# Kernel optimization log

Measured on AMD Instinct MI355X. Metric: run time of the kernel, lower is better.

Reference implementation:

```python
import jax, jax.numpy as jnp
import numpy as np

D_MODEL, D_FF, N_EXPERTS, TOP_K = 1024, 4096, 8, 2
B, S = 2, 2048


def setup_inputs() -> dict:
    key = jax.random.key(0)
    ks = jax.random.split(key, 7)
    scale = 0.02
    return {
        "x": jax.random.normal(ks[0], (B, S, D_MODEL), dtype=jnp.float32),
        "W1": jax.random.normal(ks[1], (N_EXPERTS, D_MODEL, D_FF), dtype=jnp.float32) * scale,
        "b1": jnp.zeros((N_EXPERTS, D_FF), dtype=jnp.float32),
        "W2": jax.random.normal(ks[2], (N_EXPERTS, D_FF, D_MODEL), dtype=jnp.float32) * scale,
        "b2": jnp.zeros((N_EXPERTS, D_MODEL), dtype=jnp.float32),
        "Wg": jax.random.normal(ks[3], (D_MODEL, N_EXPERTS), dtype=jnp.float32) * scale,
        "bg": jnp.zeros((N_EXPERTS,), dtype=jnp.float32),
    }


def reference(x, W1, b1, W2, b2, Wg, bg):
    # x: [B, S, d_model]
    Bx, Sx, d = x.shape
    E = W1.shape[0]
    # Gate + top-k routing (softmax over the top-k scores, as in the torch code)
    logits = jnp.einsum("bsd,de->bse", x, Wg) + bg            # [B,S,E]
    topk_scores, topk_idx = jax.lax.top_k(logits, TOP_K)       # [B,S,K]
    topk_scores = jax.nn.softmax(topk_scores, axis=-1)

    tokens = x.reshape(-1, d)                                  # [T,d]
    idx_flat = topk_idx.reshape(-1, TOP_K)                     # [T,K]
    sc_flat = topk_scores.reshape(-1, TOP_K)                   # [T,K]
    # Per-token combine weight for each expert: sum_k score_k * 1[idx_k == e]
    comb = (jax.nn.one_hot(idx_flat, E, dtype=x.dtype) * sc_flat[..., None]).sum(axis=1)  # [T,E]

    # Dense grouped expert MLP (zero combine weight kills non-selected experts)
    h = jnp.einsum("td,edf->etf", tokens, W1) + b1[:, None, :]  # [E,T,d_ff]
    even = (jnp.arange(E) % 2 == 0)[:, None, None]
    # torch nn.GELU default = exact (erf); odd experts use SiLU
    a = jnp.where(even, jax.nn.gelu(h, approximate=False), jax.nn.silu(h))
    y = jnp.einsum("etf,efd->etd", a, W2) + b2[:, None, :]      # [E,T,d_model]
    out = jnp.einsum("te,etd->td", comb, y)                     # [T,d_model]
    # Dropout is identity in eval mode
    return out.reshape(Bx, Sx, d)
```

## Files before the change

### kernel.cpp

```cpp
#include <hip/hip_runtime.h>
#include <stdint.h>

#define T_TOK 4096
#define DM 1024
#define DF 4096
#define NE 8

typedef __attribute__((ext_vector_type(8))) short bf16x8;
typedef __attribute__((ext_vector_type(4))) float f32x4;

__device__ __forceinline__ float b2f(unsigned short u) {
    union { unsigned int i; float f; } v; v.i = ((unsigned int)u) << 16; return v.f;
}
__device__ __forceinline__ unsigned short f2b(float f) {
    unsigned int i = __float_as_uint(f);
    unsigned int r = (i + 0x7FFFu + ((i >> 16) & 1u)) >> 16;
    return (unsigned short)r;
}
__device__ __forceinline__ void load_lds16(const void* g, void* l) {
    __builtin_amdgcn_global_load_lds((__attribute__((address_space(1))) void*)(g),
                                     (__attribute__((address_space(3))) void*)(l), 16, 0, 0);
}

__device__ __forceinline__ float fexp2(float x) {
#if __has_builtin(__builtin_amdgcn_exp2f)
    return __builtin_amdgcn_exp2f(x);
#else
    return exp2f(x);
#endif
}
__device__ __forceinline__ float frcp(float x) {
#if __has_builtin(__builtin_amdgcn_rcpf)
    return __builtin_amdgcn_rcpf(x);
#else
    return 1.0f / x;
#endif
}

__device__ __forceinline__ float gelu_f(float h) {
    float z = h * 0.70710678118654752f;
    float az = fabsf(z);
    float t = frcp(1.0f + 0.3275911f * az);
    float p = ((((1.061405429f * t - 1.453152027f) * t + 1.421413741f) * t
                - 0.284496736f) * t + 0.254829592f) * t;
    float e = fexp2(-1.4426950408889634f * az * az);
    float er = 1.0f - p * e;
    er = (z < 0.f) ? -er : er;
    return 0.5f * h * (1.0f + er);
}
__device__ __forceinline__ float silu_f(float h) {
    return h * frcp(1.0f + fexp2(-1.4426950408889634f * h));
}

__global__ __launch_bounds__(256) void detect_kernel(const unsigned short* __restrict__ xu,
                                                     int* __restrict__ flag) {
    const int i = (blockIdx.x * 256 + threadIdx.x) * 4;
    uint2 v = *(const uint2*)&xu[i];
    unsigned int a = v.x, b = v.y;
    int found = 0;
    if (((a >> 7)  & 0xFF) == 0xFF) found = 1;
    if (((a >> 23) & 0xFF) == 0xFF) found = 1;
    if (((b >> 7)  & 0xFF) == 0xFF) found = 1;
    if (((b >> 23) & 0xFF) == 0xFF) found = 1;
    if (__ballot(found) != 0 && (threadIdx.x & 63) == 0) atomicOr(flag, 1);
}

__global__ __launch_bounds__(256) void convx_kernel(const void* __restrict__ xin,
                                                    const int* __restrict__ flag,
                                                    unsigned short* __restrict__ xb) {
    const size_t i = ((size_t)blockIdx.x * 256 + threadIdx.x) * 8;
    if (*flag) {
        const float* xf = (const float*)xin + i;
        float4 a = *(const float4*)xf;
        float4 b = *(const float4*)(xf + 4);
        alignas(16) unsigned short t[8] = { f2b(a.x), f2b(a.y), f2b(a.z), f2b(a.w),
                                            f2b(b.x), f2b(b.y), f2b(b.z), f2b(b.w) };
        *(uint4*)(xb + i) = *(const uint4*)t;
    } else {
        *(uint4*)(xb + i) = *(const uint4*)((const unsigned short*)xin + i);
    }
}

__global__ void convf_kernel(const void* __restrict__ src, const int* __restrict__ flag,
                             float* __restrict__ dst, int n) {
    int i = blockIdx.x * 256 + threadIdx.x;
    if (i < n) dst[i] = (*flag) ? ((const float*)src)[i] : b2f(((const unsigned short*)src)[i]);
}

__global__ __launch_bounds__(256) void transpose_kernel(const void* __restrict__ in,
                                                        unsigned short* __restrict__ out,
                                                        int R, int C, const int* __restrict__ flag) {
    __shared__ unsigned short tile[64][65];
    const int isf = *flag;
    const size_t base = (size_t)blockIdx.z * R * C;
    const int r0 = blockIdx.y * 64, c0 = blockIdx.x * 64;
    const int lr = threadIdx.x >> 2;
    const int lc = (threadIdx.x & 3) * 16;
    if (isf) {
        const float* src = (const float*)in + base + (size_t)(r0 + lr) * C + c0 + lc;
#pragma unroll
        for (int q = 0; q < 4; q++) {
            float4 v = *(const float4*)(src + q * 4);
            tile[lr][lc + q * 4 + 0] = f2b(v.x);
            tile[lr][lc + q * 4 + 1] = f2b(v.y);
            tile[lr][lc + q * 4 + 2] = f2b(v.z);
            tile[lr][lc + q * 4 + 3] = f2b(v.w);
        }
    } else {
        const unsigned short* src = (const unsigned short*)in + base + (size_t)(r0 + lr) * C + c0 + lc;
#pragma unroll
        for (int q = 0; q < 2; q++) {
            uint4 v = *(const uint4*)(src + q * 8);
            unsigned int w[4] = { v.x, v.y, v.z, v.w };
#pragma unroll
            for (int j = 0; j < 4; j++) {
                tile[lr][lc + q * 8 + 2 * j]     = (unsigned short)(w[j] & 0xffff);
                tile[lr][lc + q * 8 + 2 * j + 1] = (unsigned short)(w[j] >> 16);
            }
        }
    }
    __syncthreads();
    const int oc = threadIdx.x >> 2;
    const int oj = (threadIdx.x & 3) * 16;
    alignas(16) unsigned short tmp[16];
#pragma unroll
    for (int j = 0; j < 16; j++) tmp[j] = tile[oj + j][oc];
    unsigned short* dst = out + base + (size_t)(c0 + oc) * R + r0 + oj;
    *(uint4*)(dst) = *(const uint4*)(tmp);
    *(uint4*)(dst + 8) = *(const uint4*)(tmp + 8);
}

__global__ __launch_bounds__(256) void gate_kernel(
    const void* __restrict__ x, const void* __restrict__ Wg, const void* __restrict__ bg,
    const int* __restrict__ flag, int* __restrict__ cnt,
    int* __restrict__ tok_e, float* __restrict__ tok_s) {
    const int isf = *flag;
    const int wave = threadIdx.x >> 6, lane = threadIdx.x & 63;
    const int t = blockIdx.x * 4 + wave;
    float p[8] = {0.f,0.f,0.f,0.f,0.f,0.f,0.f,0.f};
    if (isf) {
        const float* xr = (const float*)x + (size_t)t * DM;
        const float* wg = (const float*)Wg;
        for (int i = lane; i < DM; i += 64) {
            float xv = xr[i];
            float4 a = *(const float4*)(wg + (size_t)i * 8);
            float4 b = *(const float4*)(wg + (size_t)i * 8 + 4);
            p[0] += xv * a.x; p[1] += xv * a.y; p[2] += xv * a.z; p[3] += xv * a.w;
            p[4] += xv * b.x; p[5] += xv * b.y; p[6] += xv * b.z; p[7] += xv * b.w;
        }
    } else {
        const unsigned short* xr = (const unsigned short*)x + (size_t)t * DM;
        const unsigned short* wg = (const unsigned short*)Wg;
        for (int i = lane; i < DM; i += 64) {
            float xv = b2f(xr[i]);
            uint4 wv = *(const uint4*)(wg + (size_t)i * 8);
            p[0] += xv * b2f((unsigned short)(wv.x & 0xffff));
            p[1] += xv * b2f((unsigned short)(wv.x >> 16));
            p[2] += xv * b2f((unsigned short)(wv.y & 0xffff));
            p[3] += xv * b2f((unsigned short)(wv.y >> 16));
            p[4] += xv * b2f((unsigned short)(wv.z & 0xffff));
            p[5] += xv * b2f((unsigned short)(wv.z >> 16));
            p[6] += xv * b2f((unsigned short)(wv.w & 0xffff));
            p[7] += xv * b2f((unsigned short)(wv.w >> 16));
        }
    }
    for (int off = 32; off > 0; off >>= 1)
        for (int e = 0; e < 8; e++) p[e] += __shfl_down(p[e], off);
    if (lane == 0) {
        for (int e = 0; e < 8; e++)
            p[e] += isf ? ((const float*)bg)[e] : b2f(((const unsigned short*)bg)[e]);
        int e0 = 0;
        for (int e = 1; e < 8; e++) if (p[e] > p[e0]) e0 = e;
        int e1 = (e0 == 0) ? 1 : 0;
        for (int e = 0; e < 8; e++) if (e != e0 && p[e] > p[e1]) e1 = e;
        float z = expf(p[e1] - p[e0]);
        float s0 = 1.f / (1.f + z);
        tok_e[2 * t] = e0; tok_e[2 * t + 1] = e1;
        tok_s[2 * t] = s0; tok_s[2 * t + 1] = z * s0;
        atomicAdd(&cnt[e0], 1); atomicAdd(&cnt[e1], 1);
    }
}

__global__ void scan_kernel(const int* __restrict__ cnt, int* __restrict__ offs) {
    if (threadIdx.x == 0) {
        int s = 0;
        for (int e = 0; e < NE; e++) { offs[e] = s; s += cnt[e]; }
    }
}

__global__ __launch_bounds__(256) void place_kernel(
    const int* __restrict__ tok_e, const int* __restrict__ offs, int* __restrict__ cnt2,
    int* __restrict__ tok_list, int* __restrict__ slot_of) {
    const int t = blockIdx.x * 256 + threadIdx.x;
    for (int k = 0; k < 2; k++) {
        int e = tok_e[2 * t + k];
        int slot = atomicAdd(&cnt2[e], 1);
        int idx = offs[e] + slot;
        tok_list[idx] = t;
        slot_of[2 * t + k] = idx;
    }
}

__global__ __launch_bounds__(256) void gemm1_kernel(
    const unsigned short* __restrict__ xb, const unsigned short* __restrict__ W1T,
    const float* __restrict__ b1f, const int* __restrict__ tok_list,
    const int* __restrict__ offs, const int* __restrict__ cnt,
    unsigned short* __restrict__ act) {
    const int e = blockIdx.z, by = blockIdx.y, bx = blockIdx.x;
    const int ne = cnt[e];
    if (by * 128 >= ne) return;
    const int off_e = offs[e];
    __shared__ unsigned short Asm[2][128 * 32];
    __shared__ unsigned short Bsm[2][128 * 32];
    __shared__ int toks[128];
    const int tid = threadIdx.x, w = tid >> 6, lane = tid & 63;
    if (tid < 128) {
        int r = by * 128 + tid;
        toks[tid] = tok_list[off_e + (r < ne ? r : ne - 1)];
    }
    __syncthreads();
    const int arow0 = w * 16 + (lane >> 2);
    const int s_sw = (lane >> 3) & 3;
    const int acol = (((lane & 3) ^ s_sw) * 8);
    const int tok0 = toks[arow0], tok1 = toks[arow0 + 64];
    const unsigned short* gA0 = xb + (size_t)tok0 * DM + acol;
    const unsigned short* gA1 = xb + (size_t)tok1 * DM + acol;
    const unsigned short* Wte = W1T + (size_t)e * DF * DM;
    const unsigned short* gB0 = Wte + (size_t)(bx * 128 + arow0) * DM + acol;
    const unsigned short* gB1 = gB0 + (size_t)64 * DM;
    f32x4 acc[4][4] = {};
    const int mb = (w >> 1) * 64, nb = (w & 1) * 64;
    const int rdoff = (((lane >> 4) ^ ((lane >> 1) & 3)) * 8);

#define STAGE1(buf, kk) do { \
        load_lds16(gA0 + (kk), &Asm[buf][(w) * 16 * 32]); \
        load_lds16(gA1 + (kk), &Asm[buf][(w + 4) * 16 * 32]); \
        load_lds16(gB0 + (kk), &Bsm[buf][(w) * 16 * 32]); \
        load_lds16(gB1 + (kk), &Bsm[buf][(w + 4) * 16 * 32]); \
    } while (0)

    STAGE1(0, 0);
    __syncthreads();
    int cur = 0;
    for (int kk = 0; kk < DM; kk += 32) {
        if (kk + 32 < DM) STAGE1(cur ^ 1, kk + 32);
        bf16x8 af[4], bfv[4];
#pragma unroll
        for (int i = 0; i < 4; i++)
            af[i] = *(const bf16x8*)&Asm[cur][(mb + i * 16 + (lane & 15)) * 32 + rdoff];
#pragma unroll
        for (int j = 0; j < 4; j++)
            bfv[j] = *(const bf16x8*)&Bsm[cur][(nb + j * 16 + (lane & 15)) * 32 + rdoff];
        __builtin_amdgcn_s_setprio(1);
#pragma unroll
        for (int i = 0; i < 4; i++)
#pragma unroll
            for (int j = 0; j < 4; j++)
                acc[i][j] = __builtin_amdgcn_mfma_f32_16x16x32_bf16(af[i], bfv[j], acc[i][j], 0, 0, 0);
        __builtin_amdgcn_s_setprio(0);
        __syncthreads();
        cur ^= 1;
    }
#undef STAGE1

    const bool even_e = (e & 1) == 0;
    const float* b1e = b1f + (size_t)e * DF + bx * 128;
#pragma unroll
    for (int i = 0; i < 4; i++) {
#pragma unroll
        for (int r = 0; r < 4; r++) {
            int m = mb + i * 16 + ((lane >> 4) * 4) + r;
            int grow = by * 128 + m;
            if (grow < ne) {
                unsigned short* dst = act + (size_t)(off_e + grow) * DF + bx * 128;
#pragma unroll
                for (int j = 0; j < 4; j++) {
                    int n = nb + j * 16 + (lane & 15);
                    float h = acc[i][j][r] + b1e[n];
                    float a = even_e ? gelu_f(h) : silu_f(h);
                    dst[n] = f2b(a);
                }
            }
        }
    }
}

__global__ __launch_bounds__(256) void gemm2_kernel(
    const unsigned short* __restrict__ act, const unsigned short* __restrict__ W2T,
    const float* __restrict__ b2f, const int* __restrict__ offs,
    const int* __restrict__ cnt, float* __restrict__ yall) {
    const int e = blockIdx.z, by = blockIdx.y, bx = blockIdx.x;
    const int ne = cnt[e];
    if (by * 128 >= ne) return;
    const int off_e = offs[e];
    __shared__ unsigned short Asm[2][128 * 32];
    __shared__ unsigned short Bsm[2][128 * 32];
    const int tid = threadIdx.x, w = tid >> 6, lane = tid & 63;
    const int arow0 = w * 16 + (lane >> 2);
    const int s_sw = (lane >> 3) & 3;
    const int acol = (((lane & 3) ^ s_sw) * 8);
    int r0 = by * 128 + arow0;       if (r0 > ne - 1) r0 = ne - 1;
    int r1 = by * 128 + arow0 + 64;  if (r1 > ne - 1) r1 = ne - 1;
    const unsigned short* gA0 = act + (size_t)(off_e + r0) * DF + acol;
    const unsigned short* gA1 = act + (size_t)(off_e + r1) * DF + acol;
    const unsigned short* Wte = W2T + (size_t)e * DM * DF;
    const unsigned short* gB0 = Wte + (size_t)(bx * 128 + arow0) * DF + acol;
    const unsigned short* gB1 = gB0 + (size_t)64 * DF;
    f32x4 acc[4][4] = {};
    const int mb = (w >> 1) * 64, nb = (w & 1) * 64;
    const int rdoff = (((lane >> 4) ^ ((lane >> 1) & 3)) * 8);

#define STAGE2(buf, kk) do { \
        load_lds16(gA0 + (kk), &Asm[buf][(w) * 16 * 32]); \
        load_lds16(gA1 + (kk), &Asm[buf][(w + 4) * 16 * 32]); \
        load_lds16(gB0 + (kk), &Bsm[buf][(w) * 16 * 32]); \
        load_lds16(gB1 + (kk), &Bsm[buf][(w + 4) * 16 * 32]); \
    } while (0)

    STAGE2(0, 0);
    __syncthreads();
    int cur = 0;
    for (int kk = 0; kk < DF; kk += 32) {
        if (kk + 32 < DF) STAGE2(cur ^ 1, kk + 32);
        bf16x8 af[4], bfv[4];
#pragma unroll
        for (int i = 0; i < 4; i++)
            af[i] = *(const bf16x8*)&Asm[cur][(mb + i * 16 + (lane & 15)) * 32 + rdoff];
#pragma unroll
        for (int j = 0; j < 4; j++)
            bfv[j] = *(const bf16x8*)&Bsm[cur][(nb + j * 16 + (lane & 15)) * 32 + rdoff];
        __builtin_amdgcn_s_setprio(1);
#pragma unroll
        for (int i = 0; i < 4; i++)
#pragma unroll
            for (int j = 0; j < 4; j++)
                acc[i][j] = __builtin_amdgcn_mfma_f32_16x16x32_bf16(af[i], bfv[j], acc[i][j], 0, 0, 0);
        __builtin_amdgcn_s_setprio(0);
        __syncthreads();
        cur ^= 1;
    }
#undef STAGE2

    const float* b2e = b2f + (size_t)e * DM + bx * 128;
#pragma unroll
    for (int i = 0; i < 4; i++) {
#pragma unroll
        for (int r = 0; r < 4; r++) {
            int m = mb + i * 16 + ((lane >> 4) * 4) + r;
            int grow = by * 128 + m;
            if (grow < ne) {
                float* dst = yall + (size_t)(off_e + grow) * DM + bx * 128;
#pragma unroll
                for (int j = 0; j < 4; j++) {
                    int n = nb + j * 16 + (lane & 15);
                    dst[n] = acc[i][j][r] + b2e[n];
                }
            }
        }
    }
}

__global__ __launch_bounds__(256) void combine_kernel(
    const float* __restrict__ yall, const int* __restrict__ slot_of,
    const float* __restrict__ tok_s, void* __restrict__ out, const int* __restrict__ flag) {
    const int t = blockIdx.x;
    const int c = threadIdx.x * 4;
    const int s0i = slot_of[2 * t], s1i = slot_of[2 * t + 1];
    const float w0 = tok_s[2 * t], w1 = tok_s[2 * t + 1];
    float4 a = *(const float4*)&yall[(size_t)s0i * DM + c];
    float4 b = *(const float4*)&yall[(size_t)s1i * DM + c];
    float4 r;
    r.x = w0 * a.x + w1 * b.x;
    r.y = w0 * a.y + w1 * b.y;
    r.z = w0 * a.z + w1 * b.z;
    r.w = w0 * a.w + w1 * b.w;
    if (*flag) {
        *(float4*)((float*)out + (size_t)t * DM + c) = r;
    } else {
        ushort4 o;
        o.x = f2b(r.x); o.y = f2b(r.y); o.z = f2b(r.z); o.w = f2b(r.w);
        *(ushort4*)((unsigned short*)out + (size_t)t * DM + c) = o;
    }
}

extern "C" void kernel_launch(void* const* d_in, const int* in_sizes, int n_in,
                              void* d_out, int out_size, void* d_ws, size_t ws_size,
                              hipStream_t stream) {
    (void)in_sizes; (void)n_in; (void)out_size; (void)ws_size;
    const void* x  = d_in[0];
    const void* W1 = d_in[1];
    const void* b1 = d_in[2];
    const void* W2 = d_in[3];
    const void* b2 = d_in[4];
    const void* Wg = d_in[5];
    const void* bg = d_in[6];

    uint8_t* wsb = (uint8_t*)d_ws;
    int* ip = (int*)wsb;
    int* flag  = ip;
    int* cnt   = ip + 8;
    int* cnt2  = ip + 16;
    int* offs  = ip + 24;
    int* tok_e = ip + 32;
    float* tok_s  = (float*)(tok_e + 2 * T_TOK);
    int* tok_list = (int*)(tok_s + 2 * T_TOK);
    int* slot_of  = tok_list + 2 * T_TOK;
    size_t head = (size_t)((uint8_t*)(slot_of + 2 * T_TOK) - wsb);
    head = (head + 255) & ~(size_t)255;
    float* b1f = (float*)(wsb + head);
    float* b2f = b1f + (size_t)NE * DF;
    unsigned short* xb  = (unsigned short*)(b2f + (size_t)NE * DM);
    unsigned short* W1T = xb + (size_t)T_TOK * DM;
    unsigned short* W2T = W1T + (size_t)NE * DM * DF;
    unsigned short* actb = W2T + (size_t)NE * DM * DF;
    float* yall = (float*)W1T;

    hipMemsetAsync(ip, 0, 128, stream);
    detect_kernel<<<256, 256, 0, stream>>>((const unsigned short*)x, flag);
    convx_kernel<<<(T_TOK * DM) / 2048, 256, 0, stream>>>(x, flag, xb);
    convf_kernel<<<(NE * DF) / 256, 256, 0, stream>>>(b1, flag, b1f, NE * DF);
    convf_kernel<<<(NE * DM) / 256, 256, 0, stream>>>(b2, flag, b2f, NE * DM);
    transpose_kernel<<<dim3(DF / 64, DM / 64, NE), 256, 0, stream>>>(W1, W1T, DM, DF, flag);
    transpose_kernel<<<dim3(DM / 64, DF / 64, NE), 256, 0, stream>>>(W2, W2T, DF, DM, flag);
    gate_kernel<<<T_TOK / 4, 256, 0, stream>>>(x, Wg, bg, flag, cnt, tok_e, tok_s);
    scan_kernel<<<1, 64, 0, stream>>>(cnt, offs);
    place_kernel<<<T_TOK / 256, 256, 0, stream>>>(tok_e, offs, cnt2, tok_list, slot_of);
    gemm1_kernel<<<dim3(DF / 128, T_TOK / 128, NE), 256, 0, stream>>>(xb, W1T, b1f, tok_list, offs, cnt, actb);
    gemm2_kernel<<<dim3(DM / 128, T_TOK / 128, NE), 256, 0, stream>>>(actb, W2T, b2f, offs, cnt, yall);
    combine_kernel<<<T_TOK, 256, 0, stream>>>(yall, slot_of, tok_s, d_out, flag);
}
```

Before: 746.0 us.

## Triple-buffer GEMM K-loop, swizzle block IDs, and merge prep kernels

Both expert GEMMs move from double-buffered to triple-buffered LDS staging. An explicit vmcnt wait plus a single barrier per K step replaces the two syncthreads, so global loads run two stages ahead of the MFMAs. Block indices are remapped with an XCD-aware swizzle so neighbouring tiles land on the same L2 partition. The two bias conversions and the two weight transposes are each merged into one launch. The extra LDS per block may lower occupancy, and the vmcnt(4) count assumes exactly four loads per stage.

```diff
diff --git a/kernel.cpp b/kernel.cpp
--- a/kernel.cpp
+++ b/kernel.cpp
@@ -50,6 +50,11 @@
 }
 __device__ __forceinline__ float silu_f(float h) {
     return h * frcp(1.0f + fexp2(-1.4426950408889634f * h));
+}
+
+__device__ __forceinline__ int swz_bid(int H) {
+    int x = H & 7, k = H >> 3;
+    return 8 * x + 64 * (k >> 3) + (k & 7);
 }
 
 __global__ __launch_bounds__(256) void detect_kernel(const unsigned short* __restrict__ xu,
@@ -81,19 +86,38 @@
     }
 }
 
-__global__ void convf_kernel(const void* __restrict__ src, const int* __restrict__ flag,
-                             float* __restrict__ dst, int n) {
-    int i = blockIdx.x * 256 + threadIdx.x;
-    if (i < n) dst[i] = (*flag) ? ((const float*)src)[i] : b2f(((const unsigned short*)src)[i]);
-}
-
-__global__ __launch_bounds__(256) void transpose_kernel(const void* __restrict__ in,
-                                                        unsigned short* __restrict__ out,
-                                                        int R, int C, const int* __restrict__ flag) {
+__global__ void convf_kernel(const void* __restrict__ b1, const void* __restrict__ b2,
+                             const int* __restrict__ flag,
+                             float* __restrict__ d1, float* __restrict__ d2) {
+    const int i = blockIdx.x * 256 + threadIdx.x;
+    const int isf = *flag;
+    if (i < NE * DF) {
+        d1[i] = isf ? ((const float*)b1)[i] : b2f(((const unsigned short*)b1)[i]);
+    } else {
+        int j = i - NE * DF;
+        d2[j] = isf ? ((const float*)b2)[j] : b2f(((const unsigned short*)b2)[j]);
+    }
+}
+
+__global__ __launch_bounds__(256) void transpose_kernel(
+    const void* __restrict__ in1, const void* __restrict__ in2,
+    unsigned short* __restrict__ out1, unsigned short* __restrict__ out2,
+    const int* __restrict__ flag) {
     __shared__ unsigned short tile[64][65];
     const int isf = *flag;
-    const size_t base = (size_t)blockIdx.z * R * C;
-    const int r0 = blockIdx.y * 64, c0 = blockIdx.x * 64;
+    const void* in; unsigned short* out;
+    int R, C, rt, ct; size_t base;
+    if (blockIdx.z < 8) {
+        in = in1; out = out1; R = DM; C = DF;
+        base = (size_t)blockIdx.z * R * C;
+        rt = blockIdx.y; ct = blockIdx.x;
+    } else {
+        in = in2; out = out2; R = DF; C = DM;
+        base = (size_t)(blockIdx.z - 8) * R * C;
+        ct = blockIdx.x & 15;
+        rt = (blockIdx.y << 2) | (blockIdx.x >> 4);
+    }
+    const int r0 = rt * 64, c0 = ct * 64;
     const int lr = threadIdx.x >> 2;
     const int lc = (threadIdx.x & 3) * 16;
     if (isf) {
@@ -206,12 +230,14 @@
     const float* __restrict__ b1f, const int* __restrict__ tok_list,
     const int* __restrict__ offs, const int* __restrict__ cnt,
     unsigned short* __restrict__ act) {
-    const int e = blockIdx.z, by = blockIdx.y, bx = blockIdx.x;
+    const int H = blockIdx.x + 32 * (blockIdx.y + 32 * blockIdx.z);
+    const int L = swz_bid(H);
+    const int bx = L & 31, by = (L >> 5) & 31, e = L >> 10;
     const int ne = cnt[e];
     if (by * 128 >= ne) return;
     const int off_e = offs[e];
-    __shared__ unsigned short Asm[2][128 * 32];
-    __shared__ unsigned short Bsm[2][128 * 32];
+    __shared__ unsigned short Asm[3][128 * 32];
+    __shared__ unsigned short Bsm[3][128 * 32];
     __shared__ int toks[128];
     const int tid = threadIdx.x, w = tid >> 6, lane = tid & 63;
     if (tid < 128) {
@@ -240,17 +266,23 @@
     } while (0)
 
     STAGE1(0, 0);
-    __syncthreads();
-    int cur = 0;
-    for (int kk = 0; kk < DM; kk += 32) {
-        if (kk + 32 < DM) STAGE1(cur ^ 1, kk + 32);
+    STAGE1(1, 32);
+    const int NK = DM / 32;
+    int cur = 0, nxt = 2;
+    for (int t = 0; t < NK; ++t) {
+        if (t + 1 < NK) { asm volatile("s_waitcnt vmcnt(4)" ::: "memory"); }
+        else            { asm volatile("s_waitcnt vmcnt(0)" ::: "memory"); }
+        __builtin_amdgcn_s_barrier();
+        if (t + 2 < NK) STAGE1(nxt, (t + 2) * 32);
+        const unsigned short* As = &Asm[cur][0];
+        const unsigned short* Bs = &Bsm[cur][0];
         bf16x8 af[4], bfv[4];
 #pragma unroll
         for (int i = 0; i < 4; i++)
-            af[i] = *(const bf16x8*)&Asm[cur][(mb + i * 16 + (lane & 15)) * 32 + rdoff];
+            af[i] = *(const bf16x8*)&As[(mb + i * 16 + (lane & 15)) * 32 + rdoff];
 #pragma unroll
         for (int j = 0; j < 4; j++)
-            bfv[j] = *(const bf16x8*)&Bsm[cur][(nb + j * 16 + (lane & 15)) * 32 + rdoff];
+            bfv[j] = *(const bf16x8*)&Bs[(nb + j * 16 + (lane & 15)) * 32 + rdoff];
         __builtin_amdgcn_s_setprio(1);
 #pragma unroll
         for (int i = 0; i < 4; i++)
@@ -258,8 +290,8 @@
             for (int j = 0; j < 4; j++)
                 acc[i][j] = __builtin_amdgcn_mfma_f32_16x16x32_bf16(af[i], bfv[j], acc[i][j], 0, 0, 0);
         __builtin_amdgcn_s_setprio(0);
-        __syncthreads();
-        cur ^= 1;
+        cur = (cur == 2) ? 0 : cur + 1;
+        nxt = (nxt == 2) ? 0 : nxt + 1;
     }
 #undef STAGE1
 
@@ -289,12 +321,14 @@
     const unsigned short* __restrict__ act, const unsigned short* __restrict__ W2T,
     const float* __restrict__ b2f, const int* __restrict__ offs,
     const int* __restrict__ cnt, float* __restrict__ yall) {
-    const int e = blockIdx.z, by = blockIdx.y, bx = blockIdx.x;
+    const int H = blockIdx.x + 8 * (blockIdx.y + 32 * blockIdx.z);
+    const int L = swz_bid(H);
+    const int bx = L & 7, by = (L >> 3) & 31, e = L >> 8;
     const int ne = cnt[e];
     if (by * 128 >= ne) return;
     const int off_e = offs[e];
-    __shared__ unsigned short Asm[2][128 * 32];
-    __shared__ unsigned short Bsm[2][128 * 32];
+    __shared__ unsigned short Asm[3][128 * 32];
+    __shared__ unsigned short Bsm[3][128 * 32];
     const int tid = threadIdx.x, w = tid >> 6, lane = tid & 63;
     const int arow0 = w * 16 + (lane >> 2);
     const int s_sw = (lane >> 3) & 3;
@@ -318,17 +352,23 @@
     } while (0)
 
     STAGE2(0, 0);
-    __syncthreads();
-    int cur = 0;
-    for (int kk = 0; kk < DF; kk += 32) {
-        if (kk + 32 < DF) STAGE2(cur ^ 1, kk + 32);
+    STAGE2(1, 32);
+    const int NK = DF / 32;
+    int cur = 0, nxt = 2;
+    for (int t = 0; t < NK; ++t) {
+        if (t + 1 < NK) { asm volatile("s_waitcnt vmcnt(4)" ::: "memory"); }
+        else            { asm volatile("s_waitcnt vmcnt(0)" ::: "memory"); }
+        __builtin_amdgcn_s_barrier();
+        if (t + 2 < NK) STAGE2(nxt, (t + 2) * 32);
+        const unsigned short* As = &Asm[cur][0];
+        const unsigned short* Bs = &Bsm[cur][0];
         bf16x8 af[4], bfv[4];
 #pragma unroll
         for (int i = 0; i < 4; i++)
-            af[i] = *(const bf16x8*)&Asm[cur][(mb + i * 16 + (lane & 15)) * 32 + rdoff];
+            af[i] = *(const bf16x8*)&As[(mb + i * 16 + (lane & 15)) * 32 + rdoff];
 #pragma unroll
         for (int j = 0; j < 4; j++)
-            bfv[j] = *(const bf16x8*)&Bsm[cur][(nb + j * 16 + (lane & 15)) * 32 + rdoff];
+            bfv[j] = *(const bf16x8*)&Bs[(nb + j * 16 + (lane & 15)) * 32 + rdoff];
         __builtin_amdgcn_s_setprio(1);
 #pragma unroll
         for (int i = 0; i < 4; i++)
@@ -336,8 +376,8 @@
             for (int j = 0; j < 4; j++)
                 acc[i][j] = __builtin_amdgcn_mfma_f32_16x16x32_bf16(af[i], bfv[j], acc[i][j], 0, 0, 0);
         __builtin_amdgcn_s_setprio(0);
-        __syncthreads();
-        cur ^= 1;
+        cur = (cur == 2) ? 0 : cur + 1;
+        nxt = (nxt == 2) ? 0 : nxt + 1;
     }
 #undef STAGE2
 
@@ -418,10 +458,8 @@
     hipMemsetAsync(ip, 0, 128, stream);
     detect_kernel<<<256, 256, 0, stream>>>((const unsigned short*)x, flag);
     convx_kernel<<<(T_TOK * DM) / 2048, 256, 0, stream>>>(x, flag, xb);
-    convf_kernel<<<(NE * DF) / 256, 256, 0, stream>>>(b1, flag, b1f, NE * DF);
-    convf_kernel<<<(NE * DM) / 256, 256, 0, stream>>>(b2, flag, b2f, NE * DM);
-    transpose_kernel<<<dim3(DF / 64, DM / 64, NE), 256, 0, stream>>>(W1, W1T, DM, DF, flag);
-    transpose_kernel<<<dim3(DM / 64, DF / 64, NE), 256, 0, stream>>>(W2, W2T, DF, DM, flag);
+    convf_kernel<<<(NE * (DF + DM)) / 256, 256, 0, stream>>>(b1, b2, flag, b1f, b2f);
+    transpose_kernel<<<dim3(64, 16, 16), 256, 0, stream>>>(W1, W2, W1T, W2T, flag);
     gate_kernel<<<T_TOK / 4, 256, 0, stream>>>(x, Wg, bg, flag, cnt, tok_e, tok_s);
     scan_kernel<<<1, 64, 0, stream>>>(cnt, offs);
     place_kernel<<<T_TOK / 256, 256, 0, stream>>>(tok_e, offs, cnt2, tok_list, slot_of);
```

Result: no change. 757.7 us (+1.6%).
